# Kernel optimization log

Measured on AMD Instinct MI355X. Metric: run time of the kernel, lower is better.

Reference implementation:

```python
import jax, jax.numpy as jnp
import numpy as np

D = 256   # feature_dim
NQ = 512  # num query keypoints
NK = 512  # num key/value keypoints


def setup_inputs() -> dict:
    key = jax.random.key(0)
    ks = jax.random.split(key, 10)
    def w(k, shape, fan_in):
        return jax.random.normal(k, shape, dtype=jnp.float32) / np.sqrt(fan_in)
    inp = {
        "x": jax.random.normal(ks[0], (1, D, NQ), dtype=jnp.float32),
        "source": jax.random.normal(ks[1], (1, D, NK), dtype=jnp.float32),
        # MLPAttention score MLP: Conv1d(2D->D,k=1), ReLU, Conv1d(D->1,k=1)
        "w1": w(ks[2], (D, 2 * D), 2 * D),
        "b1": w(ks[3], (D,), 2 * D),
        "w2": w(ks[4], (1, D), D),
        "b2": w(ks[5], (1,), D),
        # outer MLP: Conv1d(2D->2D,k=1), ReLU, Conv1d(2D->D,k=1) with zero bias init
        "wa": w(ks[6], (2 * D, 2 * D), 2 * D),
        "ba": w(ks[7], (2 * D,), 2 * D),
        "wb": w(ks[8], (D, 2 * D), 2 * D),
        "bb": jnp.zeros((D,), dtype=jnp.float32),
    }
    return inp


def reference(x, source, w1, b1, w2, b2, wa, ba, wb, bb):
    d = x.shape[1]
    q = x[0]       # [D, nq]
    k = source[0]  # [D, nk]
    # cat((q broadcast over nk, k broadcast over nq)) then Conv1d(2D->D) is
    # equivalent to splitting w1 into query/key halves and broadcasting:
    w1q, w1k = w1[:, :d], w1[:, d:]
    aq = w1q @ q + b1[:, None]                       # [D, nq]
    ak = w1k @ k                                     # [D, nk]
    h = jax.nn.relu(aq[:, :, None] + ak[:, None, :])  # [D, nq, nk]
    scores = (jnp.einsum('d,dnm->nm', w2[0], h) + b2[0])[None]  # [1, nq, nk]
    prob = jax.nn.softmax(scores, axis=-1)
    message = jnp.einsum('bnm,bdm->bdn', prob, source)  # [1, D, nq]
    # outer MLP on cat([x, message], channel dim)
    cat = jnp.concatenate([x, message], axis=1)         # [1, 2D, nq]
    h2 = jax.nn.relu(jnp.einsum('oc,bcn->bon', wa, cat) + ba[None, :, None])
    y = jnp.einsum('oc,bcn->bon', wb, h2) + bb[None, :, None]  # [1, D, nq]
    return (y, scores)
```

## Files before the change

### kernel.cpp

```cpp
#include <hip/hip_runtime.h>
#include <hip/hip_bf16.h>

#define DD 256
#define NN 512

typedef __attribute__((ext_vector_type(8))) short short8;
typedef __attribute__((ext_vector_type(4))) float floatx4;

__device__ __forceinline__ unsigned short f2bf(float f) {
  unsigned u = __float_as_uint(f);
  u += 0x7FFFu + ((u >> 16) & 1u);
  return (unsigned short)(u >> 16);
}
__device__ __forceinline__ unsigned pack2(float a, float b) {
  return (unsigned)f2bf(a) | ((unsigned)f2bf(b) << 16);
}

__device__ __forceinline__ short8 ldfrag(const unsigned short* __restrict__ base,
                                         int row, int ld, int k, int lane) {
  return *(const short8*)(base + (row + (lane & 15)) * ld + k + ((lane >> 4) << 3));
}

__device__ __forceinline__ short8 ldfrag_f32(const float* __restrict__ base,
                                             int row, int ld, int k, int lane) {
  const float* p = base + (row + (lane & 15)) * ld + k + ((lane >> 4) << 3);
  const float4 v0 = *(const float4*)p;
  const float4 v1 = *(const float4*)(p + 4);
  short8 r;
  r[0] = (short)f2bf(v0.x); r[1] = (short)f2bf(v0.y);
  r[2] = (short)f2bf(v0.z); r[3] = (short)f2bf(v0.w);
  r[4] = (short)f2bf(v1.x); r[5] = (short)f2bf(v1.y);
  r[6] = (short)f2bf(v1.z); r[7] = (short)f2bf(v1.w);
  return r;
}

__device__ __forceinline__ short8 ldfragT_lds(const float* __restrict__ xs, int ldxs,
                                              int nrow, int k, int lane) {
  const int n = nrow + (lane & 15);
  const int kk = k + ((lane >> 4) << 3);
  short8 r;
#pragma unroll
  for (int j = 0; j < 8; ++j) r[j] = (short)f2bf(xs[(kk + j) * ldxs + n]);
  return r;
}

template <int NF>
__device__ __forceinline__ void acc_zero(floatx4 acc[NF]) {
#pragma unroll
  for (int i = 0; i < NF; ++i) {
    acc[i][0] = 0.f; acc[i][1] = 0.f; acc[i][2] = 0.f; acc[i][3] = 0.f;
  }
}

template <int NF>
__device__ __forceinline__ void ksplit_combine(floatx4 acc[NF], float* red,
                                               int wave, int lane) {
  const int W = 16 * NF;
  const int col = lane & 15;
  const int q = lane >> 4;
  if (wave > 0) {
    float* base = red + (wave - 1) * 16 * W;
#pragma unroll
    for (int nf = 0; nf < NF; ++nf)
#pragma unroll
      for (int r = 0; r < 4; ++r)
        base[(q * 4 + r) * W + nf * 16 + col] = acc[nf][r];
  }
  __syncthreads();
  if (wave == 0) {
#pragma unroll
    for (int nf = 0; nf < NF; ++nf)
#pragma unroll
      for (int r = 0; r < 4; ++r) {
        const int idx = (q * 4 + r) * W + nf * 16 + col;
        acc[nf][r] += red[idx] + red[16 * W + idx] + red[32 * W + idx];
      }
  }
}

template <int NF, bool COLBIAS, bool ROWBIAS, bool RELU, bool OUTBF>
__device__ __forceinline__ void gemm_epi(floatx4 acc[NF],
    const float* __restrict__ bias, void* __restrict__ C, int ldc,
    int m0, int n0, int lane) {
  const int col = lane & 15;
  const int q = lane >> 4;
#pragma unroll
  for (int nf = 0; nf < NF; ++nf) {
    const int n = n0 + nf * 16 + col;
    const float cb = COLBIAS ? bias[n] : 0.0f;
#pragma unroll
    for (int r = 0; r < 4; ++r) {
      const int m = m0 + q * 4 + r;
      float v = acc[nf][r] + cb + (ROWBIAS ? bias[m] : 0.0f);
      if (RELU) v = fmaxf(v, 0.0f);
      if (OUTBF) ((unsigned short*)C)[m * ldc + n] = f2bf(v);
      else       ((float*)C)[m * ldc + n] = v;
    }
  }
}

__global__ __launch_bounds__(256) void aqak_kernel(
    const float* __restrict__ x, const float* __restrict__ src,
    const float* __restrict__ w1, const float* __restrict__ b1,
    const float* __restrict__ bb,
    float* __restrict__ aq, float* __restrict__ ak, float* __restrict__ y) {
  __shared__ float xs[256][33];
  __shared__ float red[1536];

  const int tid = threadIdx.x;
  const int z = blockIdx.z;

  if (z == 2) {
    const int o = blockIdx.y * 16 + blockIdx.x;
    const float bv = bb[o];
    float2 v; v.x = bv; v.y = bv;
    *(float2*)&y[o * NN + tid * 2] = v;
    return;
  }

  const int lane = tid & 63;
  const int wave = tid >> 6;
  const int m0 = blockIdx.y * 16;
  const int n0 = blockIdx.x * 32;
  const float* in = z ? src : x;

#pragma unroll
  for (int p = 0; p < 8; ++p) {
    const int d = p * 32 + (tid >> 3);
    const int c4 = (tid & 7) * 4;
    const float4 v = *(const float4*)&in[d * NN + n0 + c4];
    xs[d][c4 + 0] = v.x; xs[d][c4 + 1] = v.y;
    xs[d][c4 + 2] = v.z; xs[d][c4 + 3] = v.w;
  }
  __syncthreads();

  floatx4 acc[2]; acc_zero<2>(acc);
#pragma unroll
  for (int kc = 0; kc < 2; ++kc) {
    const int kl = wave * 64 + kc * 32;
    short8 a = ldfrag_f32(w1, m0, NN, z * 256 + kl, lane);
#pragma unroll
    for (int nf = 0; nf < 2; ++nf) {
      short8 b = ldfragT_lds(&xs[0][0], 33, nf * 16, kl, lane);
      acc[nf] = __builtin_amdgcn_mfma_f32_16x16x32_bf16(a, b, acc[nf], 0, 0, 0);
    }
  }
  ksplit_combine<2>(acc, red, wave, lane);
  if (wave == 0) {
    if (z == 0) gemm_epi<2, false, true, false, false>(acc, b1, aq, NN, m0, n0, lane);
    else        gemm_epi<2, false, false, false, false>(acc, nullptr, ak, NN, m0, n0, lane);
  }
}

__global__ __launch_bounds__(256) void scores_kernel(
    const float* __restrict__ aq, const float* __restrict__ ak,
    const float* __restrict__ w2, const float* __restrict__ b2,
    float* __restrict__ sc) {
  __shared__ float aqs[128][32];
  __shared__ float aks[128][32];
  __shared__ float w2s[DD];

  const int tid = threadIdx.x;
  const int n0 = blockIdx.x * 32;
  const int m0 = blockIdx.y * 32;
  const int tn = tid & 31;
  const int tm4 = (tid >> 5) * 4;

  w2s[tid] = w2[tid];

  float s0 = 0.f, s1 = 0.f, s2 = 0.f, s3 = 0.f;
  for (int d0 = 0; d0 < DD; d0 += 128) {
    __syncthreads();
#pragma unroll
    for (int k = 0; k < 16; ++k) {
      const int idx = k * 256 + tid;
      const int r = idx >> 5, cc = idx & 31;
      aqs[r][cc] = aq[(d0 + r) * NN + n0 + cc];
      aks[r][cc] = ak[(d0 + r) * NN + m0 + cc];
    }
    __syncthreads();
    for (int dd = 0; dd < 128; ++dd) {
      const float w = w2s[d0 + dd];
      const float a = aqs[dd][tn];
      const float4 akv = *(const float4*)&aks[dd][tm4];
      s0 += w * fmaxf(a + akv.x, 0.f);
      s1 += w * fmaxf(a + akv.y, 0.f);
      s2 += w * fmaxf(a + akv.z, 0.f);
      s3 += w * fmaxf(a + akv.w, 0.f);
    }
  }
  const float bv = b2[0];
  float4 o; o.x = s0 + bv; o.y = s1 + bv; o.z = s2 + bv; o.w = s3 + bv;
  *(float4*)&sc[(n0 + tn) * NN + m0 + tm4] = o;
}

__global__ __launch_bounds__(256) void msgT_kernel(
    const float* __restrict__ sc, const float* __restrict__ srcf,
    unsigned short* __restrict__ msgTb) {
  __shared__ unsigned short Ap[16][520];
  __shared__ float red[1536];
  __shared__ float smax[16][16];
  __shared__ float ssum[16][16];
  __shared__ float rst[16][2];

  const int tid = threadIdx.x;
  const int lane = tid & 63;
  const int wave = tid >> 6;
  const int n0 = blockIdx.y * 16;
  const int d0 = blockIdx.x * 32;

  const int r = tid >> 4;
  const int c = tid & 15;
  float4 v[8];
  const float* rp = sc + (n0 + r) * NN + c * 4;
#pragma unroll
  for (int i = 0; i < 8; ++i) v[i] = *(const float4*)(rp + i * 64);

  float mx = -3.0e38f;
#pragma unroll
  for (int i = 0; i < 8; ++i)
    mx = fmaxf(mx, fmaxf(fmaxf(v[i].x, v[i].y), fmaxf(v[i].z, v[i].w)));
  smax[r][c] = mx;
  __syncthreads();
  if (c == 0) {
    float m2 = smax[r][0];
#pragma unroll
    for (int i = 1; i < 16; ++i) m2 = fmaxf(m2, smax[r][i]);
    rst[r][0] = m2;
  }
  __syncthreads();
  mx = rst[r][0];

  float sum = 0.f;
#pragma unroll
  for (int i = 0; i < 8; ++i) {
    v[i].x = __expf(v[i].x - mx); v[i].y = __expf(v[i].y - mx);
    v[i].z = __expf(v[i].z - mx); v[i].w = __expf(v[i].w - mx);
    sum += v[i].x + v[i].y + v[i].z + v[i].w;
  }
  ssum[r][c] = sum;
  __syncthreads();
  if (c == 0) {
    float s2 = ssum[r][0];
#pragma unroll
    for (int i = 1; i < 16; ++i) s2 += ssum[r][i];
    rst[r][1] = s2;
  }
  __syncthreads();
  const float inv = 1.0f / rst[r][1];
#pragma unroll
  for (int i = 0; i < 8; ++i) {
    *(unsigned*)&Ap[r][c * 4 + i * 64]     = pack2(v[i].x * inv, v[i].y * inv);
    *(unsigned*)&Ap[r][c * 4 + i * 64 + 2] = pack2(v[i].z * inv, v[i].w * inv);
  }
  __syncthreads();

  floatx4 acc[2]; acc_zero<2>(acc);
  const int k0w = wave * 128;
  const int arow = lane & 15;
  const int koff = (lane >> 4) << 3;
#pragma unroll
  for (int k = 0; k < 128; k += 32) {
    short8 a = *(const short8*)&Ap[arow][k0w + k + koff];
#pragma unroll
    for (int nf = 0; nf < 2; ++nf) {
      short8 b = ldfrag_f32(srcf, d0 + nf * 16, NN, k0w + k, lane);
      acc[nf] = __builtin_amdgcn_mfma_f32_16x16x32_bf16(a, b, acc[nf], 0, 0, 0);
    }
  }
  ksplit_combine<2>(acc, red, wave, lane);
  if (wave == 0)
    gemm_epi<2, false, false, false, true>(acc, nullptr, msgTb, DD, n0, d0, lane);
}

__global__ __launch_bounds__(256) void h2y_kernel(
    const float* __restrict__ x, const unsigned short* __restrict__ msgTb,
    const float* __restrict__ waf, const float* __restrict__ wbf,
    const float* __restrict__ ba, float* __restrict__ y) {
  __shared__ float xs[256][17];
  __shared__ __align__(16) unsigned short h2L[16][152];

  const int tid = threadIdx.x;
  const int lane = tid & 63;
  const int wave = tid >> 6;
  const int nt = blockIdx.x >> 2;
  const int qh = blockIdx.x & 3;
  const int n0g = nt * 16;
  const int o0 = qh * 128;

#pragma unroll
  for (int p = 0; p < 16; ++p) {
    const int d = p * 16 + (tid >> 4);
    const int n = tid & 15;
    xs[d][n] = x[d * NN + n0g + n];
  }
  __syncthreads();

  {
    floatx4 acc[2]; acc_zero<2>(acc);
    const int ow = o0 + wave * 32;
#pragma unroll
    for (int kc = 0; kc < 16; ++kc) {
      const int c0 = kc * 32;
      short8 a = (c0 < 256) ? ldfragT_lds(&xs[0][0], 17, 0, c0, lane)
                            : ldfrag(msgTb, n0g, DD, c0 - 256, lane);
#pragma unroll
      for (int nf = 0; nf < 2; ++nf) {
        short8 b = ldfrag_f32(waf, ow + nf * 16, NN, c0, lane);
        acc[nf] = __builtin_amdgcn_mfma_f32_16x16x32_bf16(a, b, acc[nf], 0, 0, 0);
      }
    }
    const int col = lane & 15, q = lane >> 4;
#pragma unroll
    for (int nf = 0; nf < 2; ++nf) {
      const int ol = wave * 32 + nf * 16 + col;
      const float cb = ba[o0 + ol];
#pragma unroll
      for (int r = 0; r < 4; ++r)
        h2L[q * 4 + r][ol] = f2bf(fmaxf(acc[nf][r] + cb, 0.f));
    }
  }
  __syncthreads();

  {
    const int brow = lane & 15;
    const int koff = (lane >> 4) << 3;
    const int col = lane & 15, q = lane >> 4;
#pragma unroll
    for (int t = 0; t < 4; ++t) {
      const int o2t = wave * 64 + t * 16;
      floatx4 acc;
      acc[0] = 0.f; acc[1] = 0.f; acc[2] = 0.f; acc[3] = 0.f;
#pragma unroll
      for (int kc = 0; kc < 4; ++kc) {
        short8 a = ldfrag_f32(wbf, o2t, NN, o0 + kc * 32, lane);
        short8 b = *(const short8*)&h2L[brow][kc * 32 + koff];
        acc = __builtin_amdgcn_mfma_f32_16x16x32_bf16(a, b, acc, 0, 0, 0);
      }
#pragma unroll
      for (int r = 0; r < 4; ++r)
        atomicAdd(&y[(o2t + q * 4 + r) * NN + n0g + col], acc[r]);
    }
  }
}

extern "C" void kernel_launch(void* const* d_in, const int* in_sizes, int n_in,
                              void* d_out, int out_size, void* d_ws, size_t ws_size,
                              hipStream_t stream) {
  (void)in_sizes; (void)n_in; (void)out_size; (void)ws_size;

  const float* x   = (const float*)d_in[0];
  const float* src = (const float*)d_in[1];
  const float* w1  = (const float*)d_in[2];
  const float* b1  = (const float*)d_in[3];
  const float* w2  = (const float*)d_in[4];
  const float* b2  = (const float*)d_in[5];
  const float* wa  = (const float*)d_in[6];
  const float* ba  = (const float*)d_in[7];
  const float* wb  = (const float*)d_in[8];
  const float* bb  = (const float*)d_in[9];

  float* y_out  = (float*)d_out;
  float* sc_out = (float*)d_out + 131072;

  char* ws = (char*)d_ws;
  float*          aq    = (float*)(ws);
  float*          ak    = (float*)(ws + (512 << 10));
  unsigned short* msgTb = (unsigned short*)(ws + (1024 << 10));

  aqak_kernel<<<dim3(16, 16, 3), 256, 0, stream>>>(x, src, w1, b1, bb, aq, ak, y_out);
  scores_kernel<<<dim3(16, 16), 256, 0, stream>>>(aq, ak, w2, b2, sc_out);
  msgT_kernel<<<dim3(8, 32), 256, 0, stream>>>(sc_out, src, msgTb);
  h2y_kernel<<<128, 256, 0, stream>>>(x, msgTb, wa, wb, ba, y_out);
}
```

Before: 108.0 us.

## Drop LDS staging of x and split h2y over more blocks with smaller output tiles

The aqak and h2y kernels no longer stage the x/source tile in shared memory. They read the transposed B fragments straight from global memory, which removes the staging loop and a barrier. h2y is relaunched as an 8x32 grid where each block computes 64 hidden channels for 16 queries (one MFMA tile per wave). That doubles the block count and halves the per-block work and LDS footprint. In exchange, global reads are strided and uncoalesced, x is re-read by more blocks, and there are twice as many atomicAdds into y.

After: 105.0 us. -2.8%, faster.

```diff
diff --git a/kernel.cpp b/kernel.cpp
--- a/kernel.cpp
+++ b/kernel.cpp
@@ -34,13 +34,13 @@
   return r;
 }
 
-__device__ __forceinline__ short8 ldfragT_lds(const float* __restrict__ xs, int ldxs,
-                                              int nrow, int k, int lane) {
-  const int n = nrow + (lane & 15);
+__device__ __forceinline__ short8 ldfragT_g(const float* __restrict__ base,
+                                            int n0, int ld, int k, int lane) {
+  const int n = n0 + (lane & 15);
   const int kk = k + ((lane >> 4) << 3);
   short8 r;
 #pragma unroll
-  for (int j = 0; j < 8; ++j) r[j] = (short)f2bf(xs[(kk + j) * ldxs + n]);
+  for (int j = 0; j < 8; ++j) r[j] = (short)f2bf(base[(kk + j) * ld + n]);
   return r;
 }
 
@@ -104,7 +104,6 @@
     const float* __restrict__ w1, const float* __restrict__ b1,
     const float* __restrict__ bb,
     float* __restrict__ aq, float* __restrict__ ak, float* __restrict__ y) {
-  __shared__ float xs[256][33];
   __shared__ float red[1536];
 
   const int tid = threadIdx.x;
@@ -124,16 +123,6 @@
   const int n0 = blockIdx.x * 32;
   const float* in = z ? src : x;
 
-#pragma unroll
-  for (int p = 0; p < 8; ++p) {
-    const int d = p * 32 + (tid >> 3);
-    const int c4 = (tid & 7) * 4;
-    const float4 v = *(const float4*)&in[d * NN + n0 + c4];
-    xs[d][c4 + 0] = v.x; xs[d][c4 + 1] = v.y;
-    xs[d][c4 + 2] = v.z; xs[d][c4 + 3] = v.w;
-  }
-  __syncthreads();
-
   floatx4 acc[2]; acc_zero<2>(acc);
 #pragma unroll
   for (int kc = 0; kc < 2; ++kc) {
@@ -141,7 +130,7 @@
     short8 a = ldfrag_f32(w1, m0, NN, z * 256 + kl, lane);
 #pragma unroll
     for (int nf = 0; nf < 2; ++nf) {
-      short8 b = ldfragT_lds(&xs[0][0], 33, nf * 16, kl, lane);
+      short8 b = ldfragT_g(in, n0 + nf * 16, NN, kl, lane);
       acc[nf] = __builtin_amdgcn_mfma_f32_16x16x32_bf16(a, b, acc[nf], 0, 0, 0);
     }
   }
@@ -277,48 +266,31 @@
     const float* __restrict__ x, const unsigned short* __restrict__ msgTb,
     const float* __restrict__ waf, const float* __restrict__ wbf,
     const float* __restrict__ ba, float* __restrict__ y) {
-  __shared__ float xs[256][17];
-  __shared__ __align__(16) unsigned short h2L[16][152];
+  __shared__ __align__(16) unsigned short h2L[16][72];
 
   const int tid = threadIdx.x;
   const int lane = tid & 63;
   const int wave = tid >> 6;
-  const int nt = blockIdx.x >> 2;
-  const int qh = blockIdx.x & 3;
-  const int n0g = nt * 16;
-  const int o0 = qh * 128;
-
-#pragma unroll
-  for (int p = 0; p < 16; ++p) {
-    const int d = p * 16 + (tid >> 4);
-    const int n = tid & 15;
-    xs[d][n] = x[d * NN + n0g + n];
-  }
-  __syncthreads();
+  const int o0 = blockIdx.x * 64;
+  const int n0g = blockIdx.y * 16;
 
   {
-    floatx4 acc[2]; acc_zero<2>(acc);
-    const int ow = o0 + wave * 32;
+    floatx4 acc;
+    acc[0] = 0.f; acc[1] = 0.f; acc[2] = 0.f; acc[3] = 0.f;
+    const int ow = o0 + wave * 16;
 #pragma unroll
     for (int kc = 0; kc < 16; ++kc) {
       const int c0 = kc * 32;
-      short8 a = (c0 < 256) ? ldfragT_lds(&xs[0][0], 17, 0, c0, lane)
+      short8 a = (c0 < 256) ? ldfragT_g(x, n0g, NN, c0, lane)
                             : ldfrag(msgTb, n0g, DD, c0 - 256, lane);
-#pragma unroll
-      for (int nf = 0; nf < 2; ++nf) {
-        short8 b = ldfrag_f32(waf, ow + nf * 16, NN, c0, lane);
-        acc[nf] = __builtin_amdgcn_mfma_f32_16x16x32_bf16(a, b, acc[nf], 0, 0, 0);
-      }
+      short8 b = ldfrag_f32(waf, ow, NN, c0, lane);
+      acc = __builtin_amdgcn_mfma_f32_16x16x32_bf16(a, b, acc, 0, 0, 0);
     }
     const int col = lane & 15, q = lane >> 4;
-#pragma unroll
-    for (int nf = 0; nf < 2; ++nf) {
-      const int ol = wave * 32 + nf * 16 + col;
-      const float cb = ba[o0 + ol];
-#pragma unroll
-      for (int r = 0; r < 4; ++r)
-        h2L[q * 4 + r][ol] = f2bf(fmaxf(acc[nf][r] + cb, 0.f));
-    }
+    const float cb = ba[o0 + wave * 16 + col];
+#pragma unroll
+    for (int r = 0; r < 4; ++r)
+      h2L[q * 4 + r][wave * 16 + col] = f2bf(fmaxf(acc[r] + cb, 0.f));
   }
   __syncthreads();
 
@@ -332,7 +304,7 @@
       floatx4 acc;
       acc[0] = 0.f; acc[1] = 0.f; acc[2] = 0.f; acc[3] = 0.f;
 #pragma unroll
-      for (int kc = 0; kc < 4; ++kc) {
+      for (int kc = 0; kc < 2; ++kc) {
         short8 a = ldfrag_f32(wbf, o2t, NN, o0 + kc * 32, lane);
         short8 b = *(const short8*)&h2L[brow][kc * 32 + koff];
         acc = __builtin_amdgcn_mfma_f32_16x16x32_bf16(a, b, acc, 0, 0, 0);
@@ -371,5 +343,5 @@
   aqak_kernel<<<dim3(16, 16, 3), 256, 0, stream>>>(x, src, w1, b1, bb, aq, ak, y_out);
   scores_kernel<<<dim3(16, 16), 256, 0, stream>>>(aq, ak, w2, b2, sc_out);
   msgT_kernel<<<dim3(8, 32), 256, 0, stream>>>(sc_out, src, msgTb);
-  h2y_kernel<<<128, 256, 0, stream>>>(x, msgTb, wa, wb, ba, y_out);
-}
+  h2y_kernel<<<dim3(8, 32), 256, 0, stream>>>(x, msgTb, wa, wb, ba, y_out);
+}
```
